# Kernel tuning notes

Measured on AMD Instinct MI355X. Metric: run time of the kernel, lower is better.

Reference implementation:

```python
import jax, jax.numpy as jnp
import numpy as np

WS = 7          # window size per spatial dim
NH = 12         # num heads
DIM = 384       # channels
HD = DIM // NH  # head dim = 32
SCALE = HD ** -0.5
N = WS * WS * WS  # 343 tokens per window
B_ = 128        # windows * batch
NW = 64         # mask windows


def _relative_position_index():
    # Faithful replica of the torch __init__ (including indexing='xy' and the
    # 3*Ws[1]-1 / 2*Ws[1]-1 stride multipliers).
    c = np.arange(WS)
    coords = np.stack(np.meshgrid(c, c, c, indexing='xy'))  # (3, WS, WS, WS)
    cf = coords.reshape(3, -1)                               # (3, N)
    rel = (cf[:, :, None] - cf[:, None, :]).transpose(1, 2, 0).astype(np.int64)
    rel = rel + (WS - 1)
    rel[..., 0] *= 3 * WS - 1
    rel[..., 1] *= 2 * WS - 1
    return rel.sum(-1).astype(np.int32)  # (N, N)


def setup_inputs() -> dict:
    key = jax.random.key(0)
    ks = jax.random.split(key, 8)
    return {
        'skip': jax.random.normal(ks[0], (B_, N, DIM), jnp.float32),
        'x_up': jax.random.normal(ks[1], (B_, N, DIM), jnp.float32),
        'pos_embed': jax.random.normal(ks[2], (B_, N, DIM), jnp.float32),
        'mask': jax.random.normal(ks[3], (NW, N, N), jnp.float32),
        'w_kv': jax.random.normal(ks[4], (2 * DIM, DIM), jnp.float32) * 0.02,
        'b_kv': jnp.zeros((2 * DIM,), jnp.float32),
        'w_proj': jax.random.normal(ks[5], (DIM, DIM), jnp.float32) * 0.02,
        'b_proj': jnp.zeros((DIM,), jnp.float32),
        'bias_table': jax.random.normal(ks[6], ((2 * WS - 1) ** 3, NH), jnp.float32) * 0.02,
        'rpi': jnp.asarray(_relative_position_index()),
    }


def reference(skip, x_up, pos_embed, mask, w_kv, b_kv, w_proj, b_proj, bias_table, rpi):
    B, Ntok, C = skip.shape
    # kv projection from skip: (B, N, 2, H, d)
    kv = (skip @ w_kv.T + b_kv).reshape(B, Ntok, 2, NH, HD)
    k = kv[:, :, 0].transpose(0, 2, 1, 3)  # (B, H, N, d)
    v = kv[:, :, 1].transpose(0, 2, 1, 3)  # (B, H, N, d)
    q = x_up.reshape(B, Ntok, NH, HD).transpose(0, 2, 1, 3) * SCALE  # (B, H, N, d)
    attn = jnp.einsum('bhnd,bhmd->bhnm', q, k)  # (B, H, N, N)
    # relative position bias gather: (N, N, H) -> (H, N, N)
    bias = bias_table[rpi.reshape(-1)].reshape(Ntok, Ntok, NH).transpose(2, 0, 1)
    attn = attn + bias[None]
    # shifted-window mask add
    nW = mask.shape[0]
    attn = attn.reshape(B // nW, nW, NH, Ntok, Ntok) + mask[None, :, None]
    attn = jax.nn.softmax(attn.reshape(B, NH, Ntok, Ntok), axis=-1)
    x = jnp.einsum('bhnm,bhmd->bnhd', attn, v).reshape(B, Ntok, C)
    x = x + pos_embed
    return x @ w_proj.T + b_proj
```

## Files before the change

### kernel.cpp

```cpp
#include <hip/hip_runtime.h>

#define NTOK 343
#define NPAD 352
#define DIM 384
#define NHEAD 12
#define HDIM 32
#define NWIN 64
#define BATCH 128
#define SCALE 0.17677669529663687f
#define NN 117649
#define MG 88
#define GSTRIDE 1372

typedef __attribute__((ext_vector_type(8))) short bf16x8;
typedef __attribute__((ext_vector_type(4))) short bf16x4;
typedef __attribute__((ext_vector_type(4))) float f32x4;
typedef __attribute__((ext_vector_type(4))) int i32x4;

static __device__ inline short f2bf(float f) {
  union { float f; unsigned u; } v; v.f = f;
  unsigned r = v.u + 0x7fffu + ((v.u >> 16) & 1u);
  return (short)(r >> 16);
}
static __device__ inline float bf2f(short s) {
  union { unsigned u; float f; } v; v.u = ((unsigned)(unsigned short)s) << 16;
  return v.f;
}
static __device__ inline int pack2(float lo, float hi) {
  return (int)((unsigned)(unsigned short)f2bf(lo) |
               ((unsigned)(unsigned short)f2bf(hi) << 16));
}
static __device__ inline int pack2rn(float lo, float hi) {
  union { float f; unsigned u; } a, b;
  a.f = lo; b.f = hi;
  unsigned au = a.u + 0x8000u;
  unsigned bu = b.u + 0x8000u;
  return (int)__builtin_amdgcn_perm(bu, au, 0x07060302u);
}
static __device__ inline short f2bfrn(float f) {
  union { float f; unsigned u; } v; v.f = f;
  return (short)((v.u + 0x8000u) >> 16);
}

#define MFMA16(a, b, c) __builtin_amdgcn_mfma_f32_16x16x32_bf16((a), (b), (c), 0, 0, 0)

__global__ __launch_bounds__(256) void bias_pk_kernel(
    const float* __restrict__ table, const int* __restrict__ rpi,
    short* __restrict__ bias_b4) {
  int idx = blockIdx.x * 256 + threadIdx.x;
  const int total = NHEAD * MG * NTOK * 4;
  if (idx >= total) return;
  int r = idx & 3;
  int t = idx >> 2;
  int q = t % NTOK;
  int u = t / NTOK;
  int g = u % MG;
  int h = u / MG;
  int m = g * 4 + r;
  bias_b4[idx] = (m < NTOK) ? f2bf(table[rpi[q * NTOK + m] * NHEAD + h]) : f2bf(-1e30f);
}

__global__ __launch_bounds__(256) void mask_pk_kernel(
    const float* __restrict__ in, short* __restrict__ mask_b4) {
  int idx = blockIdx.x * 256 + threadIdx.x;
  const int total = NWIN * MG * NTOK * 4;
  if (idx >= total) return;
  int r = idx & 3;
  int t = idx >> 2;
  int q = t % NTOK;
  int u = t / NTOK;
  int g = u % MG;
  int w = u / MG;
  int m = g * 4 + r;
  mask_b4[idx] = (m < NTOK) ? f2bf(in[(size_t)w * NN + q * NTOK + m]) : 0;
}

__global__ __launch_bounds__(256) void cvt_skip_kernel(
    const float* __restrict__ in, short* __restrict__ out, int n8) {
  int i = blockIdx.x * 256 + threadIdx.x;
  if (i >= n8) return;
  f32x4 a = *(const f32x4*)(in + (size_t)i * 8);
  f32x4 b = *(const f32x4*)(in + (size_t)i * 8 + 4);
  bf16x8 o;
#pragma unroll
  for (int j = 0; j < 4; ++j) {
    o[j] = f2bf(a[j]);
    o[j + 4] = f2bf(b[j]);
  }
  *(bf16x8*)(out + (size_t)i * 8) = o;
}

__global__ __launch_bounds__(256) void kv_proj_kernel(
    const short* __restrict__ Xbf, const float* __restrict__ W,
    const float* __restrict__ bkv, short* __restrict__ Kws,
    short* __restrict__ Vws) {
  __shared__ short As[128][40];
  __shared__ short Bs[128][40];
  const int tid = threadIdx.x;
  const int n0 = blockIdx.x * 128;
  const int m0 = blockIdx.y * 128;
  const int lane = tid & 63;
  const int wave = tid >> 6;
  const int wm = (wave >> 1) * 64;
  const int wn = (wave & 1) * 64;
  const int lr = lane & 15;
  const int lk = (lane >> 4) * 8;
  const int c4 = (tid & 7) * 4;
  const int rbase = tid >> 3;
  const int arow = tid >> 2;
  const int acol8 = (tid & 3) * 8;
  const f32x4 zero4 = {0.f, 0.f, 0.f, 0.f};

  f32x4 acc[4][4];
#pragma unroll
  for (int m = 0; m < 4; ++m)
#pragma unroll
    for (int n = 0; n < 4; ++n) acc[m][n] = zero4;

  for (int kk = 0; kk < 12; ++kk) {
    __syncthreads();
    *(bf16x8*)(&As[arow][acol8]) =
        *(const bf16x8*)(Xbf + (size_t)(m0 + arow) * DIM + kk * 32 + acol8);
    *(bf16x8*)(&As[arow + 64][acol8]) =
        *(const bf16x8*)(Xbf + (size_t)(m0 + arow + 64) * DIM + kk * 32 + acol8);
#pragma unroll
    for (int i = 0; i < 4; ++i) {
      int row = rbase + i * 32;
      f32x4 v = *(const f32x4*)(W + (size_t)(n0 + row) * DIM + kk * 32 + c4);
      bf16x4 s4;
#pragma unroll
      for (int j = 0; j < 4; ++j) s4[j] = f2bf(v[j]);
      *(bf16x4*)(&Bs[row][c4]) = s4;
    }
    __syncthreads();
    bf16x8 af[4], bf[4];
#pragma unroll
    for (int m = 0; m < 4; ++m) af[m] = *(const bf16x8*)(&As[wm + m * 16 + lr][lk]);
#pragma unroll
    for (int n = 0; n < 4; ++n) bf[n] = *(const bf16x8*)(&Bs[wn + n * 16 + lr][lk]);
#pragma unroll
    for (int m = 0; m < 4; ++m)
#pragma unroll
      for (int n = 0; n < 4; ++n) acc[m][n] = MFMA16(af[m], bf[n], acc[m][n]);
  }

  const int rq = (lane >> 4) * 4;
#pragma unroll
  for (int n = 0; n < 4; ++n) {
    int gcol = n0 + wn + n * 16 + lr;
    float bias = bkv[gcol];
    int c = (gcol >= DIM) ? (gcol - DIM) : gcol;
    int h = c >> 5;
    int hd = c & 31;
    short* dst = (gcol < DIM) ? Kws : Vws;
#pragma unroll
    for (int m = 0; m < 4; ++m) {
#pragma unroll
      for (int r = 0; r < 4; ++r) {
        int grow = m0 + wm + m * 16 + rq + r;
        int bb = grow / NTOK;
        int tok = grow - bb * NTOK;
        dst[(((size_t)bb * NHEAD + h) * NTOK + tok) * HDIM + hd] =
            f2bf(acc[m][n][r] + bias);
      }
    }
  }
}

__global__ __launch_bounds__(256, 3) void attn_kernel(
    const float* __restrict__ x_up, const short* __restrict__ mask_b4,
    const short* __restrict__ bias_b4, const short* __restrict__ Kws,
    const short* __restrict__ Vws, const float* __restrict__ pos,
    short* __restrict__ attn_out) {
  __shared__ short Ksm[NPAD][40];
  __shared__ short Vp[HDIM][NPAD + 8];
  const int bid = blockIdx.x;
  const int xcd = bid & 7;
  const int jj = bid >> 3;
  const int win = xcd * 8 + jj / 24;
  const int rep = jj - (jj / 24) * 24;
  const int h = rep % NHEAD;
  const int b = win + ((rep >= NHEAD) ? 64 : 0);
  const int tid = threadIdx.x;
  const int wave = tid >> 6;
  const int lane = tid & 63;
  const int lr = lane & 15;
  const int lg = lane >> 4;
  const int koff = lg * 8;
  const f32x4 zero4 = {0.f, 0.f, 0.f, 0.f};

  const short* Kb = Kws + ((size_t)b * NHEAD + h) * NTOK * HDIM;
  const short* Vb = Vws + ((size_t)b * NHEAD + h) * NTOK * HDIM;
  {
    const int c8 = (tid & 3) * 8;
    const int rb = tid >> 2;
    const bf16x8 z8 = {0, 0, 0, 0, 0, 0, 0, 0};
#pragma unroll
    for (int r0 = 0; r0 < 384; r0 += 64) {
      int row = r0 + rb;
      if (row < NPAD) {
        bf16x8 kv = z8;
        if (row < NTOK) kv = *(const bf16x8*)(Kb + row * HDIM + c8);
        *(bf16x8*)(&Ksm[row][c8]) = kv;
      }
    }
#pragma unroll
    for (int r0 = 0; r0 < 384; r0 += 64) {
      int row = r0 + rb;
      if (row < NPAD) {
        bf16x8 vv = z8;
        if (row < NTOK) vv = *(const bf16x8*)(Vb + row * HDIM + c8);
        int p = (row & ~31) | ((row & 12) << 1) | ((row & 16) >> 2) | (row & 3);
#pragma unroll
        for (int i = 0; i < 8; ++i) Vp[c8 + i][p] = vv[i];
      }
    }
  }
  __syncthreads();

  for (int qt = 0; qt < 6; ++qt) {
    const int q0 = qt * 64 + wave * 16;
    if (q0 >= NTOK) continue;
    const int qn = q0 + lr;
    const int qidx = (qn < NTOK) ? qn : (NTOK - 1);
    bf16x8 qf;
    {
      const float* qp = x_up + ((size_t)b * NTOK + qidx) * DIM + h * HDIM + koff;
      f32x4 v0 = *(const f32x4*)qp;
      f32x4 v1 = *(const f32x4*)(qp + 4);
#pragma unroll
      for (int i = 0; i < 4; ++i) {
        qf[i] = f2bfrn(v0[i] * SCALE);
        qf[i + 4] = f2bfrn(v1[i] * SCALE);
      }
    }
    f32x4 s[22];
    __builtin_amdgcn_s_setprio(1);
#pragma unroll
    for (int j = 0; j < 22; ++j) {
      bf16x8 kf = *(const bf16x8*)(&Ksm[j * 16 + lr][koff]);
      s[j] = MFMA16(kf, qf, zero4);
    }
    __builtin_amdgcn_s_setprio(0);
    const short* bq = bias_b4 + (size_t)h * MG * GSTRIDE + (size_t)lg * GSTRIDE +
                      qidx * 4;
    const short* mq = mask_b4 + (size_t)win * MG * GSTRIDE + (size_t)lg * GSTRIDE +
                      qidx * 4;
    float mx = -1e30f;
#pragma unroll
    for (int j = 0; j < 22; ++j) {
      bf16x4 bv = *(const bf16x4*)(bq + (size_t)j * 4 * GSTRIDE);
      bf16x4 mv = *(const bf16x4*)(mq + (size_t)j * 4 * GSTRIDE);
#pragma unroll
      for (int r = 0; r < 4; ++r) {
        float lv = s[j][r] + bf2f(bv[r]) + bf2f(mv[r]);
        s[j][r] = lv;
        mx = fmaxf(mx, lv);
      }
    }
    mx = fmaxf(mx, __shfl_xor(mx, 16));
    mx = fmaxf(mx, __shfl_xor(mx, 32));
    float sum = 0.f;
#pragma unroll
    for (int j = 0; j < 22; ++j) {
#pragma unroll
      for (int r = 0; r < 4; ++r) {
        float p = __expf(s[j][r] - mx);
        s[j][r] = p;
        sum += p;
      }
    }
    sum += __shfl_xor(sum, 16);
    sum += __shfl_xor(sum, 32);
    const float inv = 1.0f / sum;
    i32x4 up4[11];
#pragma unroll
    for (int j = 0; j < 22; ++j) {
      up4[j >> 1][(j & 1) * 2 + 0] = pack2rn(s[j][0] * inv, s[j][1] * inv);
      up4[j >> 1][(j & 1) * 2 + 1] = pack2rn(s[j][2] * inv, s[j][3] * inv);
    }

    f32x4 o0 = zero4;
    f32x4 o1 = zero4;
    __builtin_amdgcn_s_setprio(1);
#pragma unroll
    for (int kt = 0; kt < 11; ++kt) {
      bf16x8 pf = __builtin_bit_cast(bf16x8, up4[kt]);
      bf16x8 a0 = *(const bf16x8*)(&Vp[lr][kt * 32 + koff]);
      bf16x8 a1 = *(const bf16x8*)(&Vp[16 + lr][kt * 32 + koff]);
      o0 = MFMA16(a0, pf, o0);
      o1 = MFMA16(a1, pf, o1);
    }
    __builtin_amdgcn_s_setprio(0);
    if (qn < NTOK) {
      const float* pp = pos + ((size_t)b * NTOK + qn) * DIM + h * HDIM + 4 * lg;
      f32x4 p0 = *(const f32x4*)pp;
      f32x4 p1 = *(const f32x4*)(pp + 16);
      short* op = attn_out + ((size_t)b * NTOK + qn) * DIM + h * HDIM + 4 * lg;
      *(int*)(op + 0) = pack2rn(o0[0] + p0[0], o0[1] + p0[1]);
      *(int*)(op + 2) = pack2rn(o0[2] + p0[2], o0[3] + p0[3]);
      *(int*)(op + 16) = pack2rn(o1[0] + p1[0], o1[1] + p1[1]);
      *(int*)(op + 18) = pack2rn(o1[2] + p1[2], o1[3] + p1[3]);
    }
  }
}

__global__ __launch_bounds__(256) void out_proj_kernel(
    const short* __restrict__ Xa, const float* __restrict__ W,
    const float* __restrict__ bpr, float* __restrict__ out) {
  __shared__ short As[128][40];
  __shared__ short Bs[128][40];
  const int tid = threadIdx.x;
  const int n0 = blockIdx.x * 128;
  const int m0 = blockIdx.y * 128;
  const int lane = tid & 63;
  const int wave = tid >> 6;
  const int wm = (wave >> 1) * 64;
  const int wn = (wave & 1) * 64;
  const int lr = lane & 15;
  const int lk = (lane >> 4) * 8;
  const int c4 = (tid & 7) * 4;
  const int rbase = tid >> 3;
  const int arow = tid >> 2;
  const int acol8 = (tid & 3) * 8;
  const f32x4 zero4 = {0.f, 0.f, 0.f, 0.f};

  f32x4 acc[4][4];
#pragma unroll
  for (int m = 0; m < 4; ++m)
#pragma unroll
    for (int n = 0; n < 4; ++n) acc[m][n] = zero4;

  for (int kk = 0; kk < 12; ++kk) {
    __syncthreads();
    *(bf16x8*)(&As[arow][acol8]) =
        *(const bf16x8*)(Xa + (size_t)(m0 + arow) * DIM + kk * 32 + acol8);
    *(bf16x8*)(&As[arow + 64][acol8]) =
        *(const bf16x8*)(Xa + (size_t)(m0 + arow + 64) * DIM + kk * 32 + acol8);
#pragma unroll
    for (int i = 0; i < 4; ++i) {
      int row = rbase + i * 32;
      f32x4 v = *(const f32x4*)(W + (size_t)(n0 + row) * DIM + kk * 32 + c4);
      bf16x4 s4;
#pragma unroll
      for (int j = 0; j < 4; ++j) s4[j] = f2bf(v[j]);
      *(bf16x4*)(&Bs[row][c4]) = s4;
    }
    __syncthreads();
    bf16x8 af[4], bf[4];
#pragma unroll
    for (int m = 0; m < 4; ++m) af[m] = *(const bf16x8*)(&As[wm + m * 16 + lr][lk]);
#pragma unroll
    for (int n = 0; n < 4; ++n) bf[n] = *(const bf16x8*)(&Bs[wn + n * 16 + lr][lk]);
#pragma unroll
    for (int m = 0; m < 4; ++m)
#pragma unroll
      for (int n = 0; n < 4; ++n) acc[m][n] = MFMA16(af[m], bf[n], acc[m][n]);
  }

  const int rq = (lane >> 4) * 4;
#pragma unroll
  for (int n = 0; n < 4; ++n) {
    int gcol = n0 + wn + n * 16 + lr;
    float bias = bpr[gcol];
#pragma unroll
    for (int m = 0; m < 4; ++m) {
#pragma unroll
      for (int r = 0; r < 4; ++r) {
        int grow = m0 + wm + m * 16 + rq + r;
        out[(size_t)grow * DIM + gcol] = acc[m][n][r] + bias;
      }
    }
  }
}

extern "C" void kernel_launch(void* const* d_in, const int* in_sizes, int n_in,
                              void* d_out, int out_size, void* d_ws, size_t ws_size,
                              hipStream_t stream) {
  const float* skip = (const float*)d_in[0];
  const float* x_up = (const float*)d_in[1];
  const float* pos = (const float*)d_in[2];
  const float* mask = (const float*)d_in[3];
  const float* w_kv = (const float*)d_in[4];
  const float* b_kv = (const float*)d_in[5];
  const float* w_proj = (const float*)d_in[6];
  const float* b_proj = (const float*)d_in[7];
  const float* bias_table = (const float*)d_in[8];
  const int* rpi = (const int*)d_in[9];
  float* out = (float*)d_out;

  char* ws = (char*)d_ws;
  const size_t kv_bytes = (size_t)BATCH * NHEAD * NTOK * HDIM * 2;
  const size_t bias_bytes = (size_t)NHEAD * MG * NTOK * 4 * 2;
  const size_t mask_bytes = (size_t)NWIN * MG * NTOK * 4 * 2;
  short* Kws = (short*)ws;
  short* Vws = (short*)(ws + kv_bytes);
  short* bias_b4 = (short*)(ws + 2 * kv_bytes);
  short* mask_b4 = (short*)(ws + 2 * kv_bytes + bias_bytes);
  short* skip_bf = (short*)(ws + 2 * kv_bytes + bias_bytes + mask_bytes);
  short* attn_ws = skip_bf;

  const int bias_total = NHEAD * MG * NTOK * 4;
  const int mask_total = NWIN * MG * NTOK * 4;
  const int n8 = BATCH * NTOK * DIM / 8;
  bias_pk_kernel<<<dim3((bias_total + 255) / 256), dim3(256), 0, stream>>>(
      bias_table, rpi, bias_b4);
  mask_pk_kernel<<<dim3((mask_total + 255) / 256), dim3(256), 0, stream>>>(
      mask, mask_b4);
  cvt_skip_kernel<<<dim3((n8 + 255) / 256), dim3(256), 0, stream>>>(
      skip, skip_bf, n8);
  kv_proj_kernel<<<dim3(6, 343), dim3(256), 0, stream>>>(skip_bf, w_kv, b_kv,
                                                         Kws, Vws);
  attn_kernel<<<dim3(BATCH * NHEAD), dim3(256), 0, stream>>>(
      x_up, mask_b4, bias_b4, Kws, Vws, pos, attn_ws);
  out_proj_kernel<<<dim3(3, 343), dim3(256), 0, stream>>>(attn_ws, w_proj,
                                                          b_proj, out);
}
```

Measured before the change: 288.9 us.

## Use exp2 softmax with folded log2e, deferred normalization, and XCD-aware GEMM grid remap

Folds log2(e) into the query scale and the packed bias and mask tables so the softmax can use the hardware exp2 directly. Normalization by the row sum moves to the output, one multiply per output element instead of per probability, and exponentiation is fused with bf16 packing. The two projection GEMMs switch to a 1-D grid whose block ids are remapped so that consecutive tiles sharing rows land on the same XCD for L2 reuse. Unnormalized probabilities are rounded to bf16 before the PV MFMA, which slightly changes numerics.

After: 279.6 us. -3.2%, faster.

```diff
diff --git a/kernel.cpp b/kernel.cpp
--- a/kernel.cpp
+++ b/kernel.cpp
@@ -8,6 +8,8 @@
 #define NWIN 64
 #define BATCH 128
 #define SCALE 0.17677669529663687f
+#define LOG2E 1.4426950408889634f
+#define SCLG2 (0.17677669529663687f * 1.4426950408889634f)
 #define NN 117649
 #define MG 88
 #define GSTRIDE 1372
@@ -25,10 +27,6 @@
 static __device__ inline float bf2f(short s) {
   union { unsigned u; float f; } v; v.u = ((unsigned)(unsigned short)s) << 16;
   return v.f;
-}
-static __device__ inline int pack2(float lo, float hi) {
-  return (int)((unsigned)(unsigned short)f2bf(lo) |
-               ((unsigned)(unsigned short)f2bf(hi) << 16));
 }
 static __device__ inline int pack2rn(float lo, float hi) {
   union { float f; unsigned u; } a, b;
@@ -40,6 +38,9 @@
 static __device__ inline short f2bfrn(float f) {
   union { float f; unsigned u; } v; v.f = f;
   return (short)((v.u + 0x8000u) >> 16);
+}
+static __device__ inline float fexp2(float x) {
+  return __builtin_amdgcn_exp2f(x);
 }
 
 #define MFMA16(a, b, c) __builtin_amdgcn_mfma_f32_16x16x32_bf16((a), (b), (c), 0, 0, 0)
@@ -57,7 +58,8 @@
   int g = u % MG;
   int h = u / MG;
   int m = g * 4 + r;
-  bias_b4[idx] = (m < NTOK) ? f2bf(table[rpi[q * NTOK + m] * NHEAD + h]) : f2bf(-1e30f);
+  bias_b4[idx] = (m < NTOK) ? f2bf(table[rpi[q * NTOK + m] * NHEAD + h] * LOG2E)
+                            : f2bf(-1e30f);
 }
 
 __global__ __launch_bounds__(256) void mask_pk_kernel(
@@ -72,7 +74,7 @@
   int g = u % MG;
   int w = u / MG;
   int m = g * 4 + r;
-  mask_b4[idx] = (m < NTOK) ? f2bf(in[(size_t)w * NN + q * NTOK + m]) : 0;
+  mask_b4[idx] = (m < NTOK) ? f2bf(in[(size_t)w * NN + q * NTOK + m] * LOG2E) : 0;
 }
 
 __global__ __launch_bounds__(256) void cvt_skip_kernel(
@@ -96,9 +98,13 @@
     short* __restrict__ Vws) {
   __shared__ short As[128][40];
   __shared__ short Bs[128][40];
+  const int L = blockIdx.x;
+  const int xcd = L & 7;
+  const int j8 = L >> 3;
+  const int wg = ((xcd < 2) ? xcd * 258 : 516 + (xcd - 2) * 257) + j8;
+  const int n0 = (wg % 6) * 128;
+  const int m0 = (wg / 6) * 128;
   const int tid = threadIdx.x;
-  const int n0 = blockIdx.x * 128;
-  const int m0 = blockIdx.y * 128;
   const int lane = tid & 63;
   const int wave = tid >> 6;
   const int wm = (wave >> 1) * 64;
@@ -230,8 +236,8 @@
       f32x4 v1 = *(const f32x4*)(qp + 4);
 #pragma unroll
       for (int i = 0; i < 4; ++i) {
-        qf[i] = f2bfrn(v0[i] * SCALE);
-        qf[i + 4] = f2bfrn(v1[i] * SCALE);
+        qf[i] = f2bfrn(v0[i] * SCLG2);
+        qf[i + 4] = f2bfrn(v1[i] * SCLG2);
       }
     }
     f32x4 s[22];
@@ -252,33 +258,27 @@
       bf16x4 bv = *(const bf16x4*)(bq + (size_t)j * 4 * GSTRIDE);
       bf16x4 mv = *(const bf16x4*)(mq + (size_t)j * 4 * GSTRIDE);
 #pragma unroll
-      for (int r = 0; r < 4; ++r) {
-        float lv = s[j][r] + bf2f(bv[r]) + bf2f(mv[r]);
-        s[j][r] = lv;
-        mx = fmaxf(mx, lv);
-      }
+      for (int r = 0; r < 4; ++r)
+        s[j][r] += bf2f(bv[r]) + bf2f(mv[r]);
+      mx = fmaxf(mx, fmaxf(fmaxf(s[j][0], s[j][1]), fmaxf(s[j][2], s[j][3])));
     }
     mx = fmaxf(mx, __shfl_xor(mx, 16));
     mx = fmaxf(mx, __shfl_xor(mx, 32));
     float sum = 0.f;
+    i32x4 up4[11];
 #pragma unroll
     for (int j = 0; j < 22; ++j) {
-#pragma unroll
-      for (int r = 0; r < 4; ++r) {
-        float p = __expf(s[j][r] - mx);
-        s[j][r] = p;
-        sum += p;
-      }
+      float p0 = fexp2(s[j][0] - mx);
+      float p1 = fexp2(s[j][1] - mx);
+      float p2 = fexp2(s[j][2] - mx);
+      float p3 = fexp2(s[j][3] - mx);
+      sum += (p0 + p1) + (p2 + p3);
+      up4[j >> 1][(j & 1) * 2 + 0] = pack2rn(p0, p1);
+      up4[j >> 1][(j & 1) * 2 + 1] = pack2rn(p2, p3);
     }
     sum += __shfl_xor(sum, 16);
     sum += __shfl_xor(sum, 32);
     const float inv = 1.0f / sum;
-    i32x4 up4[11];
-#pragma unroll
-    for (int j = 0; j < 22; ++j) {
-      up4[j >> 1][(j & 1) * 2 + 0] = pack2rn(s[j][0] * inv, s[j][1] * inv);
-      up4[j >> 1][(j & 1) * 2 + 1] = pack2rn(s[j][2] * inv, s[j][3] * inv);
-    }
 
     f32x4 o0 = zero4;
     f32x4 o1 = zero4;
@@ -297,10 +297,10 @@
       f32x4 p0 = *(const f32x4*)pp;
       f32x4 p1 = *(const f32x4*)(pp + 16);
       short* op = attn_out + ((size_t)b * NTOK + qn) * DIM + h * HDIM + 4 * lg;
-      *(int*)(op + 0) = pack2rn(o0[0] + p0[0], o0[1] + p0[1]);
-      *(int*)(op + 2) = pack2rn(o0[2] + p0[2], o0[3] + p0[3]);
-      *(int*)(op + 16) = pack2rn(o1[0] + p1[0], o1[1] + p1[1]);
-      *(int*)(op + 18) = pack2rn(o1[2] + p1[2], o1[3] + p1[3]);
+      *(int*)(op + 0) = pack2rn(o0[0] * inv + p0[0], o0[1] * inv + p0[1]);
+      *(int*)(op + 2) = pack2rn(o0[2] * inv + p0[2], o0[3] * inv + p0[3]);
+      *(int*)(op + 16) = pack2rn(o1[0] * inv + p1[0], o1[1] * inv + p1[1]);
+      *(int*)(op + 18) = pack2rn(o1[2] * inv + p1[2], o1[3] * inv + p1[3]);
     }
   }
 }
@@ -310,9 +310,13 @@
     const float* __restrict__ bpr, float* __restrict__ out) {
   __shared__ short As[128][40];
   __shared__ short Bs[128][40];
+  const int L = blockIdx.x;
+  const int xcd = L & 7;
+  const int j8 = L >> 3;
+  const int wg = ((xcd < 5) ? xcd * 129 : 645 + (xcd - 5) * 128) + j8;
+  const int n0 = (wg % 3) * 128;
+  const int m0 = (wg / 3) * 128;
   const int tid = threadIdx.x;
-  const int n0 = blockIdx.x * 128;
-  const int m0 = blockIdx.y * 128;
   const int lane = tid & 63;
   const int wave = tid >> 6;
   const int wm = (wave >> 1) * 64;
@@ -409,10 +413,10 @@
       mask, mask_b4);
   cvt_skip_kernel<<<dim3((n8 + 255) / 256), dim3(256), 0, stream>>>(
       skip, skip_bf, n8);
-  kv_proj_kernel<<<dim3(6, 343), dim3(256), 0, stream>>>(skip_bf, w_kv, b_kv,
-                                                         Kws, Vws);
+  kv_proj_kernel<<<dim3(2058), dim3(256), 0, stream>>>(skip_bf, w_kv, b_kv,
+                                                       Kws, Vws);
   attn_kernel<<<dim3(BATCH * NHEAD), dim3(256), 0, stream>>>(
       x_up, mask_b4, bias_b4, Kws, Vws, pos, attn_ws);
-  out_proj_kernel<<<dim3(3, 343), dim3(256), 0, stream>>>(attn_ws, w_proj,
-                                                          b_proj, out);
-}
+  out_proj_kernel<<<dim3(1029), dim3(256), 0, stream>>>(attn_ws, w_proj,
+                                                        b_proj, out);
+}
```
